# Kernel optimization log

Measured on AMD Instinct MI355X. Metric: run time of the kernel, lower is better.

Reference implementation:

```python
import math
import jax, jax.numpy as jnp
import numpy as np

# dims: layers, batch, seq, hidden, heads, ffn-mult
L, B, S, D, H, FFN = 2, 4, 2048, 256, 8, 4
HD = D // H          # head dim (= head v dim, double_v_dim=False)
EPS = 1e-5
SCALE_BASE = 512


def _ln(x, w, b):
    mu = x.mean(-1, keepdims=True)
    var = x.var(-1, keepdims=True)
    return (x - mu) * jax.lax.rsqrt(var + EPS) * w + b


def _xpos_tables():
    half = HD // 2
    sv = (np.arange(0, HD, 2) + 0.4 * HD) / (1.4 * HD)            # [half]
    pos = np.arange(S, dtype=np.float64)
    scale = sv[None, :] ** (pos[:, None] / SCALE_BASE)            # [S, half]
    inv_freq = 1.0 / (10000.0 ** (np.arange(half) / half))
    ang = pos[:, None] * inv_freq[None, :]                        # [S, half]
    return (jnp.asarray(np.sin(ang), jnp.float32),
            jnp.asarray(np.cos(ang), jnp.float32),
            jnp.asarray(scale, jnp.float32))

SIN, COS, XSCALE = _xpos_tables()


def _xpos(x, downscale=False):
    # x: [B, H, S, HD]
    sc = 1.0 / XSCALE if downscale else XSCALE
    sin2 = jnp.repeat(SIN * sc, 2, axis=-1)                       # [S, HD]
    cos2 = jnp.repeat(COS * sc, 2, axis=-1)
    x1, x2 = x[..., 0::2], x[..., 1::2]
    xr = jnp.stack((-x2, x1), axis=-1).reshape(x.shape)           # rotate_every_two
    return x * cos2 + xr * sin2


def _decay_mask():
    g = 1.0 - jnp.exp(jnp.linspace(math.log(1 / 32), math.log(1 / 512), H))
    n = jnp.arange(S)[:, None]
    m = jnp.arange(S)[None, :]
    keep = n >= m
    expo = jnp.where(keep, n - m, 0).astype(jnp.float32)
    return jnp.where(keep, g[:, None, None] ** expo[None], 0.0)   # [H, S, S]

DMASK = _decay_mask()


def setup_inputs() -> dict:
    key = jax.random.key(0)
    ks = jax.random.split(key, 16)
    sc = 1.0 / D
    f32 = jnp.float32
    return {
        "X":     jax.random.normal(ks[0], (B, S, D), f32),
        "Wq":    jax.random.normal(ks[1], (L, D, D), f32) * sc,
        "Wk":    jax.random.normal(ks[2], (L, D, D), f32) * sc,
        "Wv":    jax.random.normal(ks[3], (L, D, D), f32) * sc,
        "Wg":    jax.random.normal(ks[4], (L, D, D), f32) * sc,
        "Wo":    jax.random.normal(ks[5], (L, D, D), f32) * sc,
        "gn_w":  jnp.ones((L, D), f32) + 0.02 * jax.random.normal(ks[6], (L, D), f32),
        "gn_b":  0.02 * jax.random.normal(ks[7], (L, D), f32),
        "ln1_w": jnp.ones((L, D), f32),
        "ln1_b": jnp.zeros((L, D), f32),
        "ln2_w": jnp.ones((L, D), f32),
        "ln2_b": jnp.zeros((L, D), f32),
        "w1":    jax.random.normal(ks[8], (L, D, FFN * D), f32) * 0.02,
        "b1":    0.02 * jax.random.normal(ks[9], (L, FFN * D), f32),
        "w2":    jax.random.normal(ks[10], (L, FFN * D, D), f32) * 0.02,
        "b2":    0.02 * jax.random.normal(ks[11], (L, D), f32),
        "lnf_w": jnp.ones((D,), f32),
        "lnf_b": jnp.zeros((D,), f32),
    }


def reference(X, Wq, Wk, Wv, Wg, Wo, gn_w, gn_b, ln1_w, ln1_b,
              ln2_w, ln2_b, w1, b1, w2, b2, lnf_w, lnf_b):
    x = X
    for i in range(L):
        xn = _ln(x, ln1_w[i], ln1_b[i])                           # [B,S,D]
        q = (xn @ Wq[i]).reshape(B, S, H, HD).transpose(0, 2, 1, 3)
        k = (xn @ Wk[i]).reshape(B, S, H, HD).transpose(0, 2, 1, 3)
        v = (xn @ Wv[i]).reshape(B, S, H, HD).transpose(0, 2, 1, 3)
        q = _xpos(q)
        k = _xpos(k, downscale=True)
        att = jnp.einsum('bhnd,bhmd->bhnm', q, k) * DMASK          # [B,H,S,S]
        y = jnp.einsum('bhnm,bhmd->bhnd', att, v)                  # [B,H,S,HD]
        # GroupNorm(heads, v_dim): per-(b, position, head) normalization
        mu = y.mean(-1, keepdims=True)
        var = y.var(-1, keepdims=True)
        y = (y - mu) * jax.lax.rsqrt(var + EPS)
        y = y.transpose(0, 2, 1, 3).reshape(B, S, D)               # concat heads
        y = y * gn_w[i] + gn_b[i]
        g = xn @ Wg[i]
        ret = (g * jax.nn.sigmoid(g) * y) @ Wo[i]                  # swish gate + out proj
        yres = ret + x
        yn = _ln(yres, ln2_w[i], ln2_b[i])
        f = jax.nn.gelu(yn @ w1[i] + b1[i], approximate=False) @ w2[i] + b2[i]
        x = _ln(f + yres, lnf_w, lnf_b)
    return x
```

## Files before the change

kernel.cpp:

```cpp
#include <hip/hip_runtime.h>
#include <hip/hip_bf16.h>

typedef __hip_bfloat16 bf16;
typedef unsigned short ushort_t;
typedef __attribute__((ext_vector_type(8))) short short8v;
typedef __attribute__((ext_vector_type(4))) float f32x4;
typedef __attribute__((ext_vector_type(4))) unsigned int uint4v;

#define LYR 2
#define BB 4
#define SS 2048
#define DD 256
#define HH 8
#define HDD 32
#define FFD 1024
#define MM (BB*SS)

__device__ __forceinline__ unsigned int cvtpk(float lo, float hi) {
  unsigned int r;
  asm("v_cvt_pk_bf16_f32 %0, %1, %2" : "=v"(r) : "v"(lo), "v"(hi));
  return r;
}

__device__ __forceinline__ void gload_lds16(const void* g, void* l) {
  __builtin_amdgcn_global_load_lds((const __attribute__((address_space(1))) void*)g,
                                   (__attribute__((address_space(3))) void*)l, 16, 0, 0);
}

__device__ __forceinline__ float l2g_of(int h) {
  return log2f(1.0f - expf(-3.4657359028f - 0.3960841187f * (float)h));
}

struct WDesc { const float* src; bf16* dst; int K; int N; };
struct WDescA { WDesc d[14]; float* tsn; float* tcs; float* tsc; };
__global__ __launch_bounds__(256) void wconv_k(WDescA da) {
  if (blockIdx.z == 14) {
    int i = (blockIdx.y * 32 + blockIdx.x) * 256 + threadIdx.y * 32 + threadIdx.x;
    if (i >= SS * 16) return;
    int s = i >> 4, j = i & 15;
    float sv = (2.0f * (float)j + 0.4f * (float)HDD) / (1.4f * (float)HDD);
    da.tsc[i] = powf(sv, (float)s * (1.0f / 512.0f));
    float inv_freq = powf(10000.0f, -(float)j * (1.0f / 16.0f));
    float ang = (float)s * inv_freq;
    da.tsn[i] = sinf(ang);
    da.tcs[i] = cosf(ang);
    return;
  }
  WDesc dd = da.d[blockIdx.z];
  int n0 = blockIdx.x * 32, k0 = blockIdx.y * 32;
  if (n0 >= dd.N || k0 >= dd.K) return;
  __shared__ float t[32][33];
  int tx = threadIdx.x, ty = threadIdx.y;
  #pragma unroll
  for (int i = 0; i < 32; i += 8) t[ty + i][tx] = dd.src[(size_t)(k0 + ty + i) * dd.N + n0 + tx];
  __syncthreads();
  #pragma unroll
  for (int i = 0; i < 32; i += 8) dd.dst[(size_t)(n0 + ty + i) * dd.K + k0 + tx] = __float2bfloat16(t[tx][ty + i]);
}

template<typename OT>
__global__ __launch_bounds__(256) void ln_k(const float* __restrict__ in, const float* __restrict__ w,
    const float* __restrict__ b, OT* __restrict__ out)
{
  int row = blockIdx.x, t = threadIdx.x;
  float v = in[(size_t)row * DD + t];
  __shared__ float red[4];
  float s = v;
  #pragma unroll
  for (int m = 32; m >= 1; m >>= 1) s += __shfl_xor(s, m);
  if ((t & 63) == 0) red[t >> 6] = s;
  __syncthreads();
  float mu = (red[0] + red[1] + red[2] + red[3]) * (1.0f / 256.0f);
  float d = v - mu;
  float s2 = d * d;
  #pragma unroll
  for (int m = 32; m >= 1; m >>= 1) s2 += __shfl_xor(s2, m);
  __syncthreads();
  if ((t & 63) == 0) red[t >> 6] = s2;
  __syncthreads();
  float var = (red[0] + red[1] + red[2] + red[3]) * (1.0f / 256.0f);
  float o = d * rsqrtf(var + 1e-5f) * w[t] + b[t];
  if constexpr (sizeof(OT) == 2) out[(size_t)row * DD + t] = __float2bfloat16(o);
  else                           out[(size_t)row * DD + t] = o;
}

#define STAGEG(buf, k0s) { \
    _Pragma("unroll") \
    for (int i = 0; i < BM / 32; ++i) { \
      int slot = i * 256 + tid; int row = slot >> 3, blk = slot & 7; \
      gload_lds16(Au + (size_t)(bm + row) * K + (k0s) + ((blk ^ (row & 7))) * 8, &Al[buf][slot * 8]); \
    } \
    _Pragma("unroll") \
    for (int i = 0; i < BN / 32; ++i) { \
      int slot = i * 256 + tid; int row = slot >> 3, blk = slot & 7; \
      gload_lds16(Bu + (size_t)(bn + row) * K + (k0s) + ((blk ^ (row & 7))) * 8, &Bl[buf][slot * 8]); \
    } }

enum { E_QKVG = 0, E_BGELU = 2 };

template<int BM, int BN, int K, int EPI>
__global__ __launch_bounds__(256) void mgemm_k(const bf16* __restrict__ Ag, const bf16* __restrict__ Wt,
    const float* __restrict__ bias,
    void* o0, void* o1, void* o2, void* o3, int N,
    const float* __restrict__ tsn, const float* __restrict__ tcs, const float* __restrict__ tsc)
{
  constexpr int MT = BM / 32, NT = BN / 32;
  constexpr int WMH = BM / 2, WNH = BN / 2;
  __shared__ __align__(16) ushort_t Al[2][BM * 64];
  __shared__ __align__(16) ushort_t Bl[2][BN * 64];
  const int bm = blockIdx.x * BM;
  const int bn = blockIdx.y * BN;
  const int tid = threadIdx.x;
  const int lane = tid & 63, w = tid >> 6;
  const int lg = lane >> 4, ln = lane & 15;
  const int wr = w >> 1, wc = w & 1;
  const ushort_t* Au = (const ushort_t*)Ag;
  const ushort_t* Bu = (const ushort_t*)Wt;
  f32x4 acc[MT][NT] = {};

  STAGEG(0, 0)
  asm volatile("s_waitcnt vmcnt(0)" ::: "memory");
  __builtin_amdgcn_s_barrier();

  int cur = 0;
  for (int k0 = 0; k0 < K; k0 += 64) {
    if (k0 + 64 < K) STAGEG(cur ^ 1, k0 + 64)
    #pragma unroll
    for (int kh = 0; kh < 2; ++kh) {
      short8v af[MT], bfr[NT];
      #pragma unroll
      for (int mt = 0; mt < MT; ++mt) {
        int row = wr * WMH + mt * 16 + ln;
        af[mt] = *(const short8v*)&Al[cur][row * 64 + (((kh * 4 + lg) ^ (row & 7))) * 8];
      }
      #pragma unroll
      for (int nt = 0; nt < NT; ++nt) {
        int row = wc * WNH + nt * 16 + ln;
        bfr[nt] = *(const short8v*)&Bl[cur][row * 64 + (((kh * 4 + lg) ^ (row & 7))) * 8];
      }
      #pragma unroll
      for (int mt = 0; mt < MT; ++mt)
        #pragma unroll
        for (int nt = 0; nt < NT; ++nt)
          acc[mt][nt] = __builtin_amdgcn_mfma_f32_16x16x32_bf16(af[mt], bfr[nt], acc[mt][nt], 0, 0, 0);
    }
    asm volatile("s_waitcnt vmcnt(0)" ::: "memory");
    __builtin_amdgcn_s_barrier();
    cur ^= 1;
  }

  if constexpr (EPI == E_QKVG) {
    #pragma unroll
    for (int mt = 0; mt < MT; ++mt)
      #pragma unroll
      for (int nt = 0; nt < NT; ++nt) {
        const int colbase = bn + wc * WNH + nt * 16;
        const int sec = colbase >> 8;
        const int c = (colbase & 255) + ln;
        const int grow0 = bm + wr * WMH + mt * 16 + lg * 4;
        if (sec <= 1) {
          const int jj = (c & 31) >> 1;
          const float l2g = l2g_of(c >> 5);
          #pragma unroll
          for (int r = 0; r < 4; ++r) {
            const int grow = grow0 + r;
            const int s = grow & (SS - 1);
            float v = acc[mt][nt][r];
            float pv = __shfl_xor(v, 1);
            float scv = tsc[s * 16 + jj];
            if (sec == 1) scv = 1.0f / scv;
            float ce = tcs[s * 16 + jj] * scv, se = tsn[s * 16 + jj] * scv;
            float o = (ln & 1) ? (v * ce + pv * se) : (v * ce - pv * se);
            if (sec == 0) o *= exp2f(l2g * (float)s);
            bf16* dst = (sec == 0) ? (bf16*)o0 : (bf16*)o1;
            dst[(size_t)grow * DD + c] = __float2bfloat16(o);
          }
        } else if (sec == 2) {
          const int b = grow0 >> 11, s0 = grow0 & (SS - 1);
          const int h = c >> 5, d = c & 31;
          const float nl2g = -l2g_of(h);
          float v0 = acc[mt][nt][0] * exp2f(nl2g * (float)(s0 + 0));
          float v1 = acc[mt][nt][1] * exp2f(nl2g * (float)(s0 + 1));
          float v2 = acc[mt][nt][2] * exp2f(nl2g * (float)(s0 + 2));
          float v3 = acc[mt][nt][3] * exp2f(nl2g * (float)(s0 + 3));
          uint2 pk;
          pk.x = cvtpk(v0, v1);
          pk.y = cvtpk(v2, v3);
          *(uint2*)((ushort_t*)o2 + ((size_t)(b * 8 + h) * 32 + d) * SS + s0) = pk;
        } else {
          #pragma unroll
          for (int r = 0; r < 4; ++r)
            ((float*)o3)[(size_t)(grow0 + r) * DD + c] = acc[mt][nt][r];
        }
      }
  } else {
    #pragma unroll
    for (int mt = 0; mt < MT; ++mt)
      #pragma unroll
      for (int nt = 0; nt < NT; ++nt) {
        const int gcol = bn + wc * WNH + nt * 16 + ln;
        #pragma unroll
        for (int r = 0; r < 4; ++r) {
          const int grow = bm + wr * WMH + mt * 16 + lg * 4 + r;
          float v = acc[mt][nt][r] + bias[gcol];
          v = 0.5f * v * (1.0f + erff(v * 0.70710678118654752f));
          ((bf16*)o0)[(size_t)grow * N + gcol] = __float2bfloat16(v);
        }
      }
  }
}

template<int K, int MODE, bool LAST>
__global__ __launch_bounds__(256) void mgemm_ln(const bf16* __restrict__ Ag, const bf16* __restrict__ Wt,
    const float* __restrict__ bias, const float* __restrict__ res,
    float* __restrict__ yres, bf16* __restrict__ xn, float* __restrict__ dout,
    const float* __restrict__ law, const float* __restrict__ lab,
    const float* __restrict__ lbw, const float* __restrict__ lbb)
{
  constexpr int BM = 16;
  __shared__ __align__(16) ushort_t Al[2][BM * 64];
  __shared__ __align__(16) ushort_t Bl[2][256 * 64];
  __shared__ float red[4][16][2];
  const int bm = blockIdx.x * BM;
  const int tid = threadIdx.x;
  const int lane = tid & 63, w = tid >> 6;
  const int lg = lane >> 4, ln = lane & 15;
  const ushort_t* Au = (const ushort_t*)Ag;
  const ushort_t* Bu = (const ushort_t*)Wt;
  f32x4 acc[4] = {};

  #define STAGEL(buf, k0s) { \
    if (tid < 128) { int row = tid >> 3, blk = tid & 7; \
      gload_lds16(Au + (size_t)(bm + row) * K + (k0s) + ((blk ^ (row & 7))) * 8, &Al[buf][tid * 8]); } \
    _Pragma("unroll") \
    for (int i = 0; i < 8; ++i) { \
      int slot = i * 256 + tid; int row = slot >> 3, blk = slot & 7; \
      gload_lds16(Bu + (size_t)row * K + (k0s) + ((blk ^ (row & 7))) * 8, &Bl[buf][slot * 8]); } }

  STAGEL(0, 0)
  asm volatile("s_waitcnt vmcnt(0)" ::: "memory");
  __builtin_amdgcn_s_barrier();

  int cur = 0;
  for (int k0 = 0; k0 < K; k0 += 64) {
    if (k0 + 64 < K) STAGEL(cur ^ 1, k0 + 64)
    #pragma unroll
    for (int kh = 0; kh < 2; ++kh) {
      short8v af, bfr[4];
      af = *(const short8v*)&Al[cur][ln * 64 + (((kh * 4 + lg) ^ (ln & 7))) * 8];
      #pragma unroll
      for (int nt = 0; nt < 4; ++nt) {
        int row = w * 64 + nt * 16 + ln;
        bfr[nt] = *(const short8v*)&Bl[cur][row * 64 + (((kh * 4 + lg) ^ (row & 7))) * 8];
      }
      #pragma unroll
      for (int nt = 0; nt < 4; ++nt)
        acc[nt] = __builtin_amdgcn_mfma_f32_16x16x32_bf16(af, bfr[nt], acc[nt], 0, 0, 0);
    }
    asm volatile("s_waitcnt vmcnt(0)" ::: "memory");
    __builtin_amdgcn_s_barrier();
    cur ^= 1;
  }
  #undef STAGEL

  const int row0 = lg * 4;
  float v[4][4];
  #pragma unroll
  for (int nt = 0; nt < 4; ++nt) {
    const int gcol = w * 64 + nt * 16 + ln;
    #pragma unroll
    for (int r = 0; r < 4; ++r) {
      float t = acc[nt][r];
      if constexpr (MODE == 1) t += bias[gcol];
      t += res[(size_t)(bm + row0 + r) * DD + gcol];
      v[nt][r] = t;
    }
  }
  float mu[4], rs[4];
  {
    #pragma unroll
    for (int r = 0; r < 4; ++r) {
      float s = 0.f, s2 = 0.f;
      #pragma unroll
      for (int nt = 0; nt < 4; ++nt) { s += v[nt][r]; s2 += v[nt][r] * v[nt][r]; }
      #pragma unroll
      for (int m = 8; m >= 1; m >>= 1) { s += __shfl_xor(s, m); s2 += __shfl_xor(s2, m); }
      if (ln == 0) { red[w][row0 + r][0] = s; red[w][row0 + r][1] = s2; }
    }
    __syncthreads();
    #pragma unroll
    for (int r = 0; r < 4; ++r) {
      float S  = red[0][row0 + r][0] + red[1][row0 + r][0] + red[2][row0 + r][0] + red[3][row0 + r][0];
      float S2 = red[0][row0 + r][1] + red[1][row0 + r][1] + red[2][row0 + r][1] + red[3][row0 + r][1];
      float m_ = S * (1.0f / 256.0f);
      float var = S2 * (1.0f / 256.0f) - m_ * m_;
      mu[r] = m_; rs[r] = rsqrtf(var + 1e-5f);
    }
  }

  if constexpr (MODE == 0) {
    #pragma unroll
    for (int nt = 0; nt < 4; ++nt) {
      const int gcol = w * 64 + nt * 16 + ln;
      const float lw = law[gcol], lb = lab[gcol];
      #pragma unroll
      for (int r = 0; r < 4; ++r) {
        const size_t idx = (size_t)(bm + row0 + r) * DD + gcol;
        yres[idx] = v[nt][r];
        xn[idx] = __float2bfloat16((v[nt][r] - mu[r]) * rs[r] * lw + lb);
      }
    }
  } else {
    float u[4][4];
    #pragma unroll
    for (int nt = 0; nt < 4; ++nt) {
      const int gcol = w * 64 + nt * 16 + ln;
      const float lw = law[gcol], lb = lab[gcol];
      #pragma unroll
      for (int r = 0; r < 4; ++r)
        u[nt][r] = (v[nt][r] - mu[r]) * rs[r] * lw + lb;
    }
    if constexpr (LAST) {
      #pragma unroll
      for (int nt = 0; nt < 4; ++nt) {
        const int gcol = w * 64 + nt * 16 + ln;
        #pragma unroll
        for (int r = 0; r < 4; ++r)
          dout[(size_t)(bm + row0 + r) * DD + gcol] = u[nt][r];
      }
    } else {
      __syncthreads();
      #pragma unroll
      for (int r = 0; r < 4; ++r) {
        float s = 0.f, s2 = 0.f;
        #pragma unroll
        for (int nt = 0; nt < 4; ++nt) { s += u[nt][r]; s2 += u[nt][r] * u[nt][r]; }
        #pragma unroll
        for (int m = 8; m >= 1; m >>= 1) { s += __shfl_xor(s, m); s2 += __shfl_xor(s2, m); }
        if (ln == 0) { red[w][row0 + r][0] = s; red[w][row0 + r][1] = s2; }
      }
      __syncthreads();
      float mu2[4], rs2[4];
      #pragma unroll
      for (int r = 0; r < 4; ++r) {
        float S  = red[0][row0 + r][0] + red[1][row0 + r][0] + red[2][row0 + r][0] + red[3][row0 + r][0];
        float S2 = red[0][row0 + r][1] + red[1][row0 + r][1] + red[2][row0 + r][1] + red[3][row0 + r][1];
        float m_ = S * (1.0f / 256.0f);
        float var = S2 * (1.0f / 256.0f) - m_ * m_;
        mu2[r] = m_; rs2[r] = rsqrtf(var + 1e-5f);
      }
      #pragma unroll
      for (int nt = 0; nt < 4; ++nt) {
        const int gcol = w * 64 + nt * 16 + ln;
        const float lw = lbw[gcol], lb = lbb[gcol];
        #pragma unroll
        for (int r = 0; r < 4; ++r) {
          const size_t idx = (size_t)(bm + row0 + r) * DD + gcol;
          yres[idx] = u[nt][r];
          xn[idx] = __float2bfloat16((u[nt][r] - mu2[r]) * rs2[r] * lw + lb);
        }
      }
    }
  }
}

__global__ __launch_bounds__(256) void attn_k(const bf16* __restrict__ qg, const bf16* __restrict__ kg,
    const bf16* __restrict__ vtg, const float* __restrict__ gbuf,
    const float* __restrict__ gnw, const float* __restrict__ gnb, bf16* __restrict__ ub)
{
  __shared__ __align__(16) ushort_t Kl[2][64 * 32];
  __shared__ __align__(16) ushort_t Vl[2][32 * 64];
  __shared__ __align__(16) unsigned int Pl[4][512];

  const int bh = blockIdx.x;
  const int b = bh >> 3, h = bh & (HH - 1);
  const int n0 = ((int)gridDim.y - 1 - (int)blockIdx.y) * 64;
  const int tid = threadIdx.x;
  const int w = tid >> 6, lane = tid & 63;
  const int lg = lane >> 4, ln = lane & 15;

  const size_t base = (size_t)b * SS * DD + h * HDD;
  const ushort_t* qp = (const ushort_t*)qg + base;
  const ushort_t* kp = (const ushort_t*)kg + base;
  const ushort_t* vtp = (const ushort_t*)vtg + (size_t)(b * 8 + h) * 32 * SS;

  const int n = n0 + w * 16 + ln;
  const short8v qf = *(const short8v*)(qp + (size_t)n * DD + lg * 8);

  const float l2g = l2g_of(h);
  f32x4 acc0 = {0,0,0,0}, acc1 = {0,0,0,0};

  const int Wwin = (int)(20.0f / (-l2g)) + 1;
  int m_lo = 0;
  if (n0 > Wwin) m_lo = ((n0 - Wwin) >> 6) << 6;

  const int Krow = tid >> 2, Kc8 = tid & 3;
  const int Vrow = tid >> 3, Vc8 = tid & 7;

  #define STAGE(buf, m0s) { \
    gload_lds16(kp + (size_t)((m0s) + Krow) * DD + ((Kc8 ^ (Krow & 3)) * 8), &Kl[buf][tid * 8]); \
    gload_lds16(vtp + (size_t)Vrow * SS + (m0s) + ((Vc8 ^ (Vrow & 7)) * 8), &Vl[buf][tid * 8]); }

  STAGE(0, m_lo)
  asm volatile("s_waitcnt vmcnt(0)" ::: "memory");
  __builtin_amdgcn_s_barrier();

  int cur = 0;
  for (int m0 = m_lo; m0 <= n0; m0 += 64) {
    if (m0 < n0) STAGE(cur ^ 1, m0 + 64)
    const bool diag = (m0 == n0);
    __builtin_amdgcn_s_setprio(1);
    #pragma unroll
    for (int mt = 0; mt < 4; ++mt) {
      const int krow = mt * 16 + ln;
      short8v kf = *(const short8v*)&Kl[cur][krow * 32 + ((lg ^ (krow & 3)) << 3)];
      f32x4 z = {0,0,0,0};
      f32x4 pa = __builtin_amdgcn_mfma_f32_16x16x32_bf16(kf, qf, z, 0, 0, 0);
      float v0 = pa[0], v1 = pa[1], v2 = pa[2], v3 = pa[3];
      if (diag) {
        const int m = n0 + mt * 16 + lg * 4;
        v0 = (n < m)     ? 0.f : v0;
        v1 = (n < m + 1) ? 0.f : v1;
        v2 = (n < m + 2) ? 0.f : v2;
        v3 = (n < m + 3) ? 0.f : v3;
      }
      uint2 pk;
      pk.x = cvtpk(v0, v1);
      pk.y = cvtpk(v2, v3);
      const int blk = (mt * 2 + (lg >> 1)) ^ (ln & 7);
      *(uint2*)&Pl[w][ln * 32 + blk * 4 + (lg & 1) * 2] = pk;
    }
    #pragma unroll
    for (int hh = 0; hh < 2; ++hh) {
      const int pblk = (hh * 4 + lg) ^ (ln & 7);
      uint4v pw = *(const uint4v*)&Pl[w][ln * 32 + pblk * 4];
      short8v pf = __builtin_bit_cast(short8v, pw);
      #pragma unroll
      for (int dt = 0; dt < 2; ++dt) {
        const int d = dt * 16 + ln;
        short8v vf = *(const short8v*)&Vl[cur][d * 64 + (((hh * 4 + lg) ^ (d & 7)) << 3)];
        if (dt == 0) acc0 = __builtin_amdgcn_mfma_f32_16x16x32_bf16(vf, pf, acc0, 0, 0, 0);
        else         acc1 = __builtin_amdgcn_mfma_f32_16x16x32_bf16(vf, pf, acc1, 0, 0, 0);
      }
    }
    __builtin_amdgcn_s_setprio(0);
    asm volatile("s_waitcnt vmcnt(0)" ::: "memory");
    __builtin_amdgcn_s_barrier();
    cur ^= 1;
  }
  #undef STAGE

  float gwv[8], gbv[8];
  #pragma unroll
  for (int dt = 0; dt < 2; ++dt) {
    f32x4 a = *(const f32x4*)&gnw[h * 32 + dt * 16 + lg * 4];
    f32x4 c = *(const f32x4*)&gnb[h * 32 + dt * 16 + lg * 4];
    #pragma unroll
    for (int r = 0; r < 4; ++r) { gwv[dt * 4 + r] = a[r]; gbv[dt * 4 + r] = c[r]; }
  }
  float s = 0.f;
  #pragma unroll
  for (int r = 0; r < 4; ++r) s += acc0[r] + acc1[r];
  s += __shfl_xor(s, 16); s += __shfl_xor(s, 32);
  const float mu = s * (1.0f / 32.0f);
  float s2 = 0.f;
  #pragma unroll
  for (int r = 0; r < 4; ++r) { float d0 = acc0[r] - mu, d1 = acc1[r] - mu; s2 += d0 * d0 + d1 * d1; }
  s2 += __shfl_xor(s2, 16); s2 += __shfl_xor(s2, 32);
  const float rs = rsqrtf(s2 * (1.0f / 32.0f) + 1e-5f);
  const size_t rowoff = ((size_t)b * SS + n) * DD + h * 32;
  #pragma unroll
  for (int dt = 0; dt < 2; ++dt) {
    f32x4 yv = dt ? acc1 : acc0;
    f32x4 gv = *(const f32x4*)&gbuf[rowoff + dt * 16 + lg * 4];
    float o0, o1, o2, o3;
    {
      float yn0 = (yv[0] - mu) * rs * gwv[dt * 4 + 0] + gbv[dt * 4 + 0];
      float yn1 = (yv[1] - mu) * rs * gwv[dt * 4 + 1] + gbv[dt * 4 + 1];
      float yn2 = (yv[2] - mu) * rs * gwv[dt * 4 + 2] + gbv[dt * 4 + 2];
      float yn3 = (yv[3] - mu) * rs * gwv[dt * 4 + 3] + gbv[dt * 4 + 3];
      o0 = gv[0] / (1.0f + expf(-gv[0])) * yn0;
      o1 = gv[1] / (1.0f + expf(-gv[1])) * yn1;
      o2 = gv[2] / (1.0f + expf(-gv[2])) * yn2;
      o3 = gv[3] / (1.0f + expf(-gv[3])) * yn3;
    }
    uint2 pk;
    pk.x = cvtpk(o0, o1);
    pk.y = cvtpk(o2, o3);
    *(uint2*)((ushort_t*)ub + rowoff + dt * 16 + lg * 4) = pk;
  }
}

extern "C" void kernel_launch(void* const* d_in, const int* in_sizes, int n_in,
                              void* d_out, int out_size, void* d_ws, size_t ws_size,
                              hipStream_t stream)
{
  const float* X    = (const float*)d_in[0];
  const float* Wq   = (const float*)d_in[1];
  const float* Wk   = (const float*)d_in[2];
  const float* Wv   = (const float*)d_in[3];
  const float* Wg   = (const float*)d_in[4];
  const float* Wo   = (const float*)d_in[5];
  const float* gnw  = (const float*)d_in[6];
  const float* gnb  = (const float*)d_in[7];
  const float* ln1w = (const float*)d_in[8];
  const float* ln1b = (const float*)d_in[9];
  const float* ln2w = (const float*)d_in[10];
  const float* ln2b = (const float*)d_in[11];
  const float* w1   = (const float*)d_in[12];
  const float* b1   = (const float*)d_in[13];
  const float* w2   = (const float*)d_in[14];
  const float* b2   = (const float*)d_in[15];
  const float* lnfw = (const float*)d_in[16];
  const float* lnfb = (const float*)d_in[17];

  char* p = (char*)d_ws;
  const size_t AF  = (size_t)MM * DD * sizeof(float);
  const size_t ABF = (size_t)MM * DD * sizeof(bf16);
  bf16*  xn   = (bf16*)p;  p += ABF;
  bf16*  qb   = (bf16*)p;  p += ABF;
  bf16*  kb   = (bf16*)p;  p += ABF;
  bf16*  vT   = (bf16*)p;  p += ABF;
  bf16*  ub   = (bf16*)p;  p += ABF;
  float* gbuf = (float*)p; p += AF;
  float* yres = (float*)p; p += AF;
  bf16*  wqkvgt = (bf16*)p; p += (size_t)2 * 1024 * 256 * sizeof(bf16);
  bf16*  wot    = (bf16*)p; p += (size_t)2 * 256 * 256 * sizeof(bf16);
  bf16*  w1t    = (bf16*)p; p += (size_t)2 * 1024 * 256 * sizeof(bf16);
  bf16*  w2t    = (bf16*)p; p += (size_t)2 * 256 * 1024 * sizeof(bf16);
  float* tsn  = (float*)p; p += SS * 16 * sizeof(float);
  float* tcs  = (float*)p; p += SS * 16 * sizeof(float);
  float* tsc  = (float*)p; p += SS * 16 * sizeof(float);
  bf16*  h1   = qb;

  {
    WDescA da;
    for (int l = 0; l < 2; ++l) {
      da.d[l * 7 + 0] = { Wq + (size_t)l * 65536, wqkvgt + (size_t)l * 262144 + 0 * 65536, 256, 256 };
      da.d[l * 7 + 1] = { Wk + (size_t)l * 65536, wqkvgt + (size_t)l * 262144 + 1 * 65536, 256, 256 };
      da.d[l * 7 + 2] = { Wv + (size_t)l * 65536, wqkvgt + (size_t)l * 262144 + 2 * 65536, 256, 256 };
      da.d[l * 7 + 3] = { Wg + (size_t)l * 65536, wqkvgt + (size_t)l * 262144 + 3 * 65536, 256, 256 };
      da.d[l * 7 + 4] = { Wo + (size_t)l * 65536, wot + (size_t)l * 65536, 256, 256 };
      da.d[l * 7 + 5] = { w1 + (size_t)l * 262144, w1t + (size_t)l * 262144, 256, 1024 };
      da.d[l * 7 + 6] = { w2 + (size_t)l * 262144, w2t + (size_t)l * 262144, 1024, 256 };
    }
    da.tsn = tsn; da.tcs = tcs; da.tsc = tsc;
    wconv_k<<<dim3(32, 32, 15), dim3(32, 8), 0, stream>>>(da);
  }

  ln_k<bf16><<<dim3(MM), 256, 0, stream>>>(X, ln1w, ln1b, xn);

  for (int l = 0; l < LYR; ++l) {
    mgemm_k<64, 128, DD, E_QKVG><<<dim3(MM / 64, 1024 / 128), 256, 0, stream>>>(
        xn, wqkvgt + (size_t)l * 262144, nullptr, qb, kb, vT, gbuf, 1024, tsn, tcs, tsc);
    attn_k<<<dim3(BB * HH, SS / 64), 256, 0, stream>>>(qb, kb, vT, gbuf, gnw + l * DD, gnb + l * DD, ub);
    mgemm_ln<DD, 0, false><<<dim3(MM / 16), 256, 0, stream>>>(
        ub, wot + (size_t)l * 65536, nullptr, (l == 0) ? X : yres, yres, xn, nullptr,
        ln2w + l * DD, ln2b + l * DD, nullptr, nullptr);
    mgemm_k<64, 128, DD, E_BGELU><<<dim3(MM / 64, FFD / 128), 256, 0, stream>>>(
        xn, w1t + (size_t)l * 262144, b1 + l * FFD, h1, nullptr, nullptr, nullptr, FFD, tsn, tcs, tsc);
    if (l == LYR - 1) {
      mgemm_ln<FFD, 1, true><<<dim3(MM / 16), 256, 0, stream>>>(
          h1, w2t + (size_t)l * 262144, b2 + l * DD, yres, nullptr, nullptr, (float*)d_out,
          lnfw, lnfb, nullptr, nullptr);
    } else {
      mgemm_ln<FFD, 1, false><<<dim3(MM / 16), 256, 0, stream>>>(
          h1, w2t + (size_t)l * 262144, b2 + l * DD, yres, yres, xn, nullptr,
          lnfw, lnfb, ln1w + (l + 1) * DD, ln1b + (l + 1) * DD);
    }
  }
}
```

Before: 200.5 us.

## Fuse out-projection, LN2, FFN up/GELU/down and final LNs into one kernel

New measurement: 200.6 us. Within noise of the previous version (+0.0%).

```diff
diff --git a/kernel.cpp b/kernel.cpp
--- a/kernel.cpp
+++ b/kernel.cpp
@@ -21,6 +21,7 @@
   asm("v_cvt_pk_bf16_f32 %0, %1, %2" : "=v"(r) : "v"(lo), "v"(hi));
   return r;
 }
+__device__ __forceinline__ ushort_t f2b1(float x) { return (ushort_t)cvtpk(x, x); }
 
 __device__ __forceinline__ void gload_lds16(const void* g, void* l) {
   __builtin_amdgcn_global_load_lds((const __attribute__((address_space(1))) void*)g,
@@ -96,12 +97,11 @@
       gload_lds16(Bu + (size_t)(bn + row) * K + (k0s) + ((blk ^ (row & 7))) * 8, &Bl[buf][slot * 8]); \
     } }
 
-enum { E_QKVG = 0, E_BGELU = 2 };
+enum { E_QKVG = 0 };
 
 template<int BM, int BN, int K, int EPI>
 __global__ __launch_bounds__(256) void mgemm_k(const bf16* __restrict__ Ag, const bf16* __restrict__ Wt,
-    const float* __restrict__ bias,
-    void* o0, void* o1, void* o2, void* o3, int N,
+    void* o0, void* o1, void* o2, void* o3,
     const float* __restrict__ tsn, const float* __restrict__ tcs, const float* __restrict__ tsc)
 {
   constexpr int MT = BM / 32, NT = BN / 32;
@@ -149,219 +149,297 @@
     cur ^= 1;
   }
 
-  if constexpr (EPI == E_QKVG) {
-    #pragma unroll
-    for (int mt = 0; mt < MT; ++mt)
-      #pragma unroll
-      for (int nt = 0; nt < NT; ++nt) {
-        const int colbase = bn + wc * WNH + nt * 16;
-        const int sec = colbase >> 8;
-        const int c = (colbase & 255) + ln;
-        const int grow0 = bm + wr * WMH + mt * 16 + lg * 4;
-        if (sec <= 1) {
-          const int jj = (c & 31) >> 1;
-          const float l2g = l2g_of(c >> 5);
-          #pragma unroll
-          for (int r = 0; r < 4; ++r) {
-            const int grow = grow0 + r;
-            const int s = grow & (SS - 1);
-            float v = acc[mt][nt][r];
-            float pv = __shfl_xor(v, 1);
-            float scv = tsc[s * 16 + jj];
-            if (sec == 1) scv = 1.0f / scv;
-            float ce = tcs[s * 16 + jj] * scv, se = tsn[s * 16 + jj] * scv;
-            float o = (ln & 1) ? (v * ce + pv * se) : (v * ce - pv * se);
-            if (sec == 0) o *= exp2f(l2g * (float)s);
-            bf16* dst = (sec == 0) ? (bf16*)o0 : (bf16*)o1;
-            dst[(size_t)grow * DD + c] = __float2bfloat16(o);
-          }
-        } else if (sec == 2) {
-          const int b = grow0 >> 11, s0 = grow0 & (SS - 1);
-          const int h = c >> 5, d = c & 31;
-          const float nl2g = -l2g_of(h);
-          float v0 = acc[mt][nt][0] * exp2f(nl2g * (float)(s0 + 0));
-          float v1 = acc[mt][nt][1] * exp2f(nl2g * (float)(s0 + 1));
-          float v2 = acc[mt][nt][2] * exp2f(nl2g * (float)(s0 + 2));
-          float v3 = acc[mt][nt][3] * exp2f(nl2g * (float)(s0 + 3));
-          uint2 pk;
-          pk.x = cvtpk(v0, v1);
-          pk.y = cvtpk(v2, v3);
-          *(uint2*)((ushort_t*)o2 + ((size_t)(b * 8 + h) * 32 + d) * SS + s0) = pk;
-        } else {
-          #pragma unroll
-          for (int r = 0; r < 4; ++r)
-            ((float*)o3)[(size_t)(grow0 + r) * DD + c] = acc[mt][nt][r];
-        }
-      }
-  } else {
-    #pragma unroll
-    for (int mt = 0; mt < MT; ++mt)
-      #pragma unroll
-      for (int nt = 0; nt < NT; ++nt) {
-        const int gcol = bn + wc * WNH + nt * 16 + ln;
+  #pragma unroll
+  for (int mt = 0; mt < MT; ++mt)
+    #pragma unroll
+    for (int nt = 0; nt < NT; ++nt) {
+      const int colbase = bn + wc * WNH + nt * 16;
+      const int sec = colbase >> 8;
+      const int c = (colbase & 255) + ln;
+      const int grow0 = bm + wr * WMH + mt * 16 + lg * 4;
+      if (sec <= 1) {
+        const int jj = (c & 31) >> 1;
+        const float l2g = l2g_of(c >> 5);
         #pragma unroll
         for (int r = 0; r < 4; ++r) {
-          const int grow = bm + wr * WMH + mt * 16 + lg * 4 + r;
-          float v = acc[mt][nt][r] + bias[gcol];
-          v = 0.5f * v * (1.0f + erff(v * 0.70710678118654752f));
-          ((bf16*)o0)[(size_t)grow * N + gcol] = __float2bfloat16(v);
+          const int grow = grow0 + r;
+          const int s = grow & (SS - 1);
+          float v = acc[mt][nt][r];
+          float pv = __shfl_xor(v, 1);
+          float scv = tsc[s * 16 + jj];
+          if (sec == 1) scv = 1.0f / scv;
+          float ce = tcs[s * 16 + jj] * scv, se = tsn[s * 16 + jj] * scv;
+          float o = (ln & 1) ? (v * ce + pv * se) : (v * ce - pv * se);
+          if (sec == 0) o *= exp2f(l2g * (float)s);
+          bf16* dst = (sec == 0) ? (bf16*)o0 : (bf16*)o1;
+          dst[(size_t)grow * DD + c] = __float2bfloat16(o);
         }
-      }
-  }
-}
-
-template<int K, int MODE, bool LAST>
-__global__ __launch_bounds__(256) void mgemm_ln(const bf16* __restrict__ Ag, const bf16* __restrict__ Wt,
-    const float* __restrict__ bias, const float* __restrict__ res,
+      } else if (sec == 2) {
+        const int b = grow0 >> 11, s0 = grow0 & (SS - 1);
+        const int h = c >> 5, d = c & 31;
+        const float nl2g = -l2g_of(h);
+        float v0 = acc[mt][nt][0] * exp2f(nl2g * (float)(s0 + 0));
+        float v1 = acc[mt][nt][1] * exp2f(nl2g * (float)(s0 + 1));
+        float v2 = acc[mt][nt][2] * exp2f(nl2g * (float)(s0 + 2));
+        float v3 = acc[mt][nt][3] * exp2f(nl2g * (float)(s0 + 3));
+        uint2 pk;
+        pk.x = cvtpk(v0, v1);
+        pk.y = cvtpk(v2, v3);
+        *(uint2*)((ushort_t*)o2 + ((size_t)(b * 8 + h) * 32 + d) * SS + s0) = pk;
+      } else {
+        #pragma unroll
+        for (int r = 0; r < 4; ++r)
+          ((float*)o3)[(size_t)(grow0 + r) * DD + c] = acc[mt][nt][r];
+      }
+    }
+}
+
+template<bool LAST>
+__global__ __launch_bounds__(256) void ffn_mega(
+    const bf16* __restrict__ ubg, const bf16* __restrict__ wotg,
+    const bf16* __restrict__ w1tg, const bf16* __restrict__ w2tg,
+    const float* __restrict__ b1v, const float* __restrict__ b2v,
+    const float* __restrict__ resin,
     float* __restrict__ yres, bf16* __restrict__ xn, float* __restrict__ dout,
-    const float* __restrict__ law, const float* __restrict__ lab,
-    const float* __restrict__ lbw, const float* __restrict__ lbb)
+    const float* __restrict__ l2w, const float* __restrict__ l2b,
+    const float* __restrict__ lfw, const float* __restrict__ lfb,
+    const float* __restrict__ l1w, const float* __restrict__ l1b)
 {
-  constexpr int BM = 16;
-  __shared__ __align__(16) ushort_t Al[2][BM * 64];
-  __shared__ __align__(16) ushort_t Bl[2][256 * 64];
-  __shared__ float red[4][16][2];
-  const int bm = blockIdx.x * BM;
+  __shared__ __align__(16) ushort_t Bs[2][256 * 64];
+  __shared__ __align__(16) ushort_t AX[4096];
+  __shared__ __align__(16) ushort_t Us[4096];
+
+  const int bm = blockIdx.x * 16;
   const int tid = threadIdx.x;
   const int lane = tid & 63, w = tid >> 6;
   const int lg = lane >> 4, ln = lane & 15;
-  const ushort_t* Au = (const ushort_t*)Ag;
-  const ushort_t* Bu = (const ushort_t*)Wt;
-  f32x4 acc[4] = {};
-
-  #define STAGEL(buf, k0s) { \
-    if (tid < 128) { int row = tid >> 3, blk = tid & 7; \
-      gload_lds16(Au + (size_t)(bm + row) * K + (k0s) + ((blk ^ (row & 7))) * 8, &Al[buf][tid * 8]); } \
+  const int row0 = lg * 4;
+  const ushort_t* ubu  = (const ushort_t*)ubg;
+  const ushort_t* wotu = (const ushort_t*)wotg;
+  const ushort_t* w1tu = (const ushort_t*)w1tg;
+  const ushort_t* w2tu = (const ushort_t*)w2tg;
+  float* red = (float*)Us;
+
+  float resv[4][4];
+  #pragma unroll
+  for (int nt = 0; nt < 4; ++nt) {
+    const int gcol = w * 64 + nt * 16 + ln;
+    #pragma unroll
+    for (int r = 0; r < 4; ++r)
+      resv[nt][r] = resin[(size_t)(bm + row0 + r) * DD + gcol];
+  }
+
+  #define STAGEB(buf, base, stride, koff) { \
     _Pragma("unroll") \
     for (int i = 0; i < 8; ++i) { \
       int slot = i * 256 + tid; int row = slot >> 3, blk = slot & 7; \
-      gload_lds16(Bu + (size_t)row * K + (k0s) + ((blk ^ (row & 7))) * 8, &Bl[buf][slot * 8]); } }
-
-  STAGEL(0, 0)
-  asm volatile("s_waitcnt vmcnt(0)" ::: "memory");
-  __builtin_amdgcn_s_barrier();
-
+      gload_lds16((base) + (size_t)row * (stride) + (koff) + ((blk ^ (row & 7))) * 8, &Bs[buf][slot * 8]); \
+    } }
+  #define STAGEA(buf, koff) { \
+    if (tid < 128) { int row = tid >> 3, blk = tid & 7; \
+      gload_lds16(ubu + (size_t)(bm + row) * DD + (koff) + ((blk ^ (row & 7))) * 8, &AX[(buf) * 1024 + tid * 8]); } }
+  #define DRAIN asm volatile("s_waitcnt vmcnt(0)" ::: "memory"); __builtin_amdgcn_s_barrier();
+
+  STAGEA(0, 0)
+  STAGEB(0, wotu, 256, 0)
+  DRAIN
   int cur = 0;
-  for (int k0 = 0; k0 < K; k0 += 64) {
-    if (k0 + 64 < K) STAGEL(cur ^ 1, k0 + 64)
+
+  f32x4 accw[4] = {};
+  #pragma unroll
+  for (int s = 0; s < 4; ++s) {
+    if (s < 3) { STAGEA(cur ^ 1, (s + 1) * 64) STAGEB(cur ^ 1, wotu, 256, (s + 1) * 64) }
+    else       { STAGEB(cur ^ 1, w1tu, 256, 0) }
     #pragma unroll
     for (int kh = 0; kh < 2; ++kh) {
-      short8v af, bfr[4];
-      af = *(const short8v*)&Al[cur][ln * 64 + (((kh * 4 + lg) ^ (ln & 7))) * 8];
+      short8v af = *(const short8v*)&AX[cur * 1024 + ln * 64 + (((kh * 4 + lg) ^ (ln & 7))) * 8];
       #pragma unroll
       for (int nt = 0; nt < 4; ++nt) {
         int row = w * 64 + nt * 16 + ln;
-        bfr[nt] = *(const short8v*)&Bl[cur][row * 64 + (((kh * 4 + lg) ^ (row & 7))) * 8];
-      }
-      #pragma unroll
-      for (int nt = 0; nt < 4; ++nt)
-        acc[nt] = __builtin_amdgcn_mfma_f32_16x16x32_bf16(af, bfr[nt], acc[nt], 0, 0, 0);
-    }
-    asm volatile("s_waitcnt vmcnt(0)" ::: "memory");
-    __builtin_amdgcn_s_barrier();
+        short8v bf_ = *(const short8v*)&Bs[cur][row * 64 + (((kh * 4 + lg) ^ (row & 7))) * 8];
+        accw[nt] = __builtin_amdgcn_mfma_f32_16x16x32_bf16(af, bf_, accw[nt], 0, 0, 0);
+      }
+    }
+    DRAIN
     cur ^= 1;
   }
-  #undef STAGEL
-
-  const int row0 = lg * 4;
+
   float v[4][4];
+  #pragma unroll
+  for (int nt = 0; nt < 4; ++nt)
+    #pragma unroll
+    for (int r = 0; r < 4; ++r) v[nt][r] = accw[nt][r] + resv[nt][r];
+  float mu[4], rsg[4];
+  {
+    #pragma unroll
+    for (int r = 0; r < 4; ++r) {
+      float s1 = 0.f, s2 = 0.f;
+      #pragma unroll
+      for (int nt = 0; nt < 4; ++nt) { s1 += v[nt][r]; s2 += v[nt][r] * v[nt][r]; }
+      #pragma unroll
+      for (int m = 8; m >= 1; m >>= 1) { s1 += __shfl_xor(s1, m); s2 += __shfl_xor(s2, m); }
+      if (ln == 0) { red[(w * 16 + row0 + r) * 2] = s1; red[(w * 16 + row0 + r) * 2 + 1] = s2; }
+    }
+    __syncthreads();
+    #pragma unroll
+    for (int r = 0; r < 4; ++r) {
+      float S = 0.f, S2 = 0.f;
+      #pragma unroll
+      for (int ww = 0; ww < 4; ++ww) { S += red[(ww * 16 + row0 + r) * 2]; S2 += red[(ww * 16 + row0 + r) * 2 + 1]; }
+      float m_ = S * (1.0f / 256.0f);
+      mu[r] = m_; rsg[r] = rsqrtf(S2 * (1.0f / 256.0f) - m_ * m_ + 1e-5f);
+    }
+  }
+  __syncthreads();
   #pragma unroll
   for (int nt = 0; nt < 4; ++nt) {
     const int gcol = w * 64 + nt * 16 + ln;
+    const float lwv = l2w[gcol], lbv = l2b[gcol];
+    const int off = nt * 16 + ln, blk = off >> 3, sub = off & 7;
     #pragma unroll
     for (int r = 0; r < 4; ++r) {
-      float t = acc[nt][r];
-      if constexpr (MODE == 1) t += bias[gcol];
-      t += res[(size_t)(bm + row0 + r) * DD + gcol];
-      v[nt][r] = t;
-    }
-  }
-  float mu[4], rs[4];
+      const int row = row0 + r;
+      float xv = (v[nt][r] - mu[r]) * rsg[r] * lwv + lbv;
+      AX[row * 256 + w * 64 + ((blk ^ (row & 7)) << 3) + sub] = f2b1(xv);
+    }
+  }
+  __syncthreads();
+
+  f32x4 acc2[4] = {};
+  #pragma unroll
+  for (int c = 0; c < 4; ++c) {
+    f32x4 acc1[4] = {};
+    #pragma unroll
+    for (int s = 0; s < 4; ++s) {
+      if (s < 3) { STAGEB(cur ^ 1, w1tu + (size_t)c * 65536, 256, (s + 1) * 64) }
+      else       { STAGEB(cur ^ 1, w2tu + c * 256, 1024, 0) }
+      #pragma unroll
+      for (int kh = 0; kh < 2; ++kh) {
+        short8v af = *(const short8v*)&AX[ln * 256 + s * 64 + (((kh * 4 + lg) ^ (ln & 7))) * 8];
+        #pragma unroll
+        for (int nt = 0; nt < 4; ++nt) {
+          int row = w * 64 + nt * 16 + ln;
+          short8v bf_ = *(const short8v*)&Bs[cur][row * 64 + (((kh * 4 + lg) ^ (row & 7))) * 8];
+          acc1[nt] = __builtin_amdgcn_mfma_f32_16x16x32_bf16(af, bf_, acc1[nt], 0, 0, 0);
+        }
+      }
+      DRAIN
+      cur ^= 1;
+    }
+    #pragma unroll
+    for (int nt = 0; nt < 4; ++nt) {
+      const int gcol1 = c * 256 + w * 64 + nt * 16 + ln;
+      const float bb = b1v[gcol1];
+      const int off = nt * 16 + ln, blk = off >> 3, sub = off & 7;
+      #pragma unroll
+      for (int r = 0; r < 4; ++r) {
+        const int row = row0 + r;
+        float t = acc1[nt][r] + bb;
+        t = 0.5f * t * (1.0f + erff(t * 0.70710678118654752f));
+        Us[row * 256 + w * 64 + ((blk ^ (row & 7)) << 3) + sub] = f2b1(t);
+      }
+    }
+    __syncthreads();
+    #pragma unroll
+    for (int s = 0; s < 4; ++s) {
+      if (s < 3)      { STAGEB(cur ^ 1, w2tu + c * 256, 1024, (s + 1) * 64) }
+      else if (c < 3) { STAGEB(cur ^ 1, w1tu + (size_t)(c + 1) * 65536, 256, 0) }
+      #pragma unroll
+      for (int kh = 0; kh < 2; ++kh) {
+        short8v af = *(const short8v*)&Us[ln * 256 + s * 64 + (((kh * 4 + lg) ^ (ln & 7))) * 8];
+        #pragma unroll
+        for (int nt = 0; nt < 4; ++nt) {
+          int row = w * 64 + nt * 16 + ln;
+          short8v bf_ = *(const short8v*)&Bs[cur][row * 64 + (((kh * 4 + lg) ^ (row & 7))) * 8];
+          acc2[nt] = __builtin_amdgcn_mfma_f32_16x16x32_bf16(af, bf_, acc2[nt], 0, 0, 0);
+        }
+      }
+      DRAIN
+      cur ^= 1;
+    }
+  }
+
+  float f[4][4];
+  #pragma unroll
+  for (int nt = 0; nt < 4; ++nt) {
+    const int gcol = w * 64 + nt * 16 + ln;
+    const float bb = b2v[gcol];
+    #pragma unroll
+    for (int r = 0; r < 4; ++r) f[nt][r] = acc2[nt][r] + bb + v[nt][r];
+  }
   {
     #pragma unroll
     for (int r = 0; r < 4; ++r) {
-      float s = 0.f, s2 = 0.f;
-      #pragma unroll
-      for (int nt = 0; nt < 4; ++nt) { s += v[nt][r]; s2 += v[nt][r] * v[nt][r]; }
-      #pragma unroll
-      for (int m = 8; m >= 1; m >>= 1) { s += __shfl_xor(s, m); s2 += __shfl_xor(s2, m); }
-      if (ln == 0) { red[w][row0 + r][0] = s; red[w][row0 + r][1] = s2; }
+      float s1 = 0.f, s2 = 0.f;
+      #pragma unroll
+      for (int nt = 0; nt < 4; ++nt) { s1 += f[nt][r]; s2 += f[nt][r] * f[nt][r]; }
+      #pragma unroll
+      for (int m = 8; m >= 1; m >>= 1) { s1 += __shfl_xor(s1, m); s2 += __shfl_xor(s2, m); }
+      if (ln == 0) { red[(w * 16 + row0 + r) * 2] = s1; red[(w * 16 + row0 + r) * 2 + 1] = s2; }
     }
     __syncthreads();
     #pragma unroll
     for (int r = 0; r < 4; ++r) {
-      float S  = red[0][row0 + r][0] + red[1][row0 + r][0] + red[2][row0 + r][0] + red[3][row0 + r][0];
-      float S2 = red[0][row0 + r][1] + red[1][row0 + r][1] + red[2][row0 + r][1] + red[3][row0 + r][1];
+      float S = 0.f, S2 = 0.f;
+      #pragma unroll
+      for (int ww = 0; ww < 4; ++ww) { S += red[(ww * 16 + row0 + r) * 2]; S2 += red[(ww * 16 + row0 + r) * 2 + 1]; }
       float m_ = S * (1.0f / 256.0f);
-      float var = S2 * (1.0f / 256.0f) - m_ * m_;
-      mu[r] = m_; rs[r] = rsqrtf(var + 1e-5f);
-    }
-  }
-
-  if constexpr (MODE == 0) {
+      mu[r] = m_; rsg[r] = rsqrtf(S2 * (1.0f / 256.0f) - m_ * m_ + 1e-5f);
+    }
+  }
+  float u[4][4];
+  #pragma unroll
+  for (int nt = 0; nt < 4; ++nt) {
+    const int gcol = w * 64 + nt * 16 + ln;
+    const float lwv = lfw[gcol], lbv = lfb[gcol];
+    #pragma unroll
+    for (int r = 0; r < 4; ++r)
+      u[nt][r] = (f[nt][r] - mu[r]) * rsg[r] * lwv + lbv;
+  }
+  if constexpr (LAST) {
     #pragma unroll
     for (int nt = 0; nt < 4; ++nt) {
       const int gcol = w * 64 + nt * 16 + ln;
-      const float lw = law[gcol], lb = lab[gcol];
+      #pragma unroll
+      for (int r = 0; r < 4; ++r)
+        dout[(size_t)(bm + row0 + r) * DD + gcol] = u[nt][r];
+    }
+  } else {
+    __syncthreads();
+    #pragma unroll
+    for (int r = 0; r < 4; ++r) {
+      float s1 = 0.f, s2 = 0.f;
+      #pragma unroll
+      for (int nt = 0; nt < 4; ++nt) { s1 += u[nt][r]; s2 += u[nt][r] * u[nt][r]; }
+      #pragma unroll
+      for (int m = 8; m >= 1; m >>= 1) { s1 += __shfl_xor(s1, m); s2 += __shfl_xor(s2, m); }
+      if (ln == 0) { red[(w * 16 + row0 + r) * 2] = s1; red[(w * 16 + row0 + r) * 2 + 1] = s2; }
+    }
+    __syncthreads();
+    float mu2[4], rs2[4];
+    #pragma unroll
+    for (int r = 0; r < 4; ++r) {
+      float S = 0.f, S2 = 0.f;
+      #pragma unroll
+      for (int ww = 0; ww < 4; ++ww) { S += red[(ww * 16 + row0 + r) * 2]; S2 += red[(ww * 16 + row0 + r) * 2 + 1]; }
+      float m_ = S * (1.0f / 256.0f);
+      mu2[r] = m_; rs2[r] = rsqrtf(S2 * (1.0f / 256.0f) - m_ * m_ + 1e-5f);
+    }
+    #pragma unroll
+    for (int nt = 0; nt < 4; ++nt) {
+      const int gcol = w * 64 + nt * 16 + ln;
+      const float lwv = l1w[gcol], lbv = l1b[gcol];
       #pragma unroll
       for (int r = 0; r < 4; ++r) {
         const size_t idx = (size_t)(bm + row0 + r) * DD + gcol;
-        yres[idx] = v[nt][r];
-        xn[idx] = __float2bfloat16((v[nt][r] - mu[r]) * rs[r] * lw + lb);
-      }
-    }
-  } else {
-    float u[4][4];
-    #pragma unroll
-    for (int nt = 0; nt < 4; ++nt) {
-      const int gcol = w * 64 + nt * 16 + ln;
-      const float lw = law[gcol], lb = lab[gcol];
-      #pragma unroll
-      for (int r = 0; r < 4; ++r)
-        u[nt][r] = (v[nt][r] - mu[r]) * rs[r] * lw + lb;
-    }
-    if constexpr (LAST) {
-      #pragma unroll
-      for (int nt = 0; nt < 4; ++nt) {
-        const int gcol = w * 64 + nt * 16 + ln;
-        #pragma unroll
-        for (int r = 0; r < 4; ++r)
-          dout[(size_t)(bm + row0 + r) * DD + gcol] = u[nt][r];
-      }
-    } else {
-      __syncthreads();
-      #pragma unroll
-      for (int r = 0; r < 4; ++r) {
-        float s = 0.f, s2 = 0.f;
-        #pragma unroll
-        for (int nt = 0; nt < 4; ++nt) { s += u[nt][r]; s2 += u[nt][r] * u[nt][r]; }
-        #pragma unroll
-        for (int m = 8; m >= 1; m >>= 1) { s += __shfl_xor(s, m); s2 += __shfl_xor(s2, m); }
-        if (ln == 0) { red[w][row0 + r][0] = s; red[w][row0 + r][1] = s2; }
-      }
-      __syncthreads();
-      float mu2[4], rs2[4];
-      #pragma unroll
-      for (int r = 0; r < 4; ++r) {
-        float S  = red[0][row0 + r][0] + red[1][row0 + r][0] + red[2][row0 + r][0] + red[3][row0 + r][0];
-        float S2 = red[0][row0 + r][1] + red[1][row0 + r][1] + red[2][row0 + r][1] + red[3][row0 + r][1];
-        float m_ = S * (1.0f / 256.0f);
-        float var = S2 * (1.0f / 256.0f) - m_ * m_;
-        mu2[r] = m_; rs2[r] = rsqrtf(var + 1e-5f);
-      }
-      #pragma unroll
-      for (int nt = 0; nt < 4; ++nt) {
-        const int gcol = w * 64 + nt * 16 + ln;
-        const float lw = lbw[gcol], lb = lbb[gcol];
-        #pragma unroll
-        for (int r = 0; r < 4; ++r) {
-          const size_t idx = (size_t)(bm + row0 + r) * DD + gcol;
-          yres[idx] = u[nt][r];
-          xn[idx] = __float2bfloat16((u[nt][r] - mu2[r]) * rs2[r] * lw + lb);
-        }
-      }
-    }
-  }
+        yres[idx] = u[nt][r];
+        xn[idx] = __float2bfloat16((u[nt][r] - mu2[r]) * rs2[r] * lwv + lbv);
+      }
+    }
+  }
+  #undef STAGEB
+  #undef STAGEA
+  #undef DRAIN
 }
 
 __global__ __launch_bounds__(256) void attn_k(const bf16* __restrict__ qg, const bf16* __restrict__ kg,
@@ -531,7 +609,6 @@
   float* tsn  = (float*)p; p += SS * 16 * sizeof(float);
   float* tcs  = (float*)p; p += SS * 16 * sizeof(float);
   float* tsc  = (float*)p; p += SS * 16 * sizeof(float);
-  bf16*  h1   = qb;
 
   {
     WDescA da;
@@ -552,21 +629,20 @@
 
   for (int l = 0; l < LYR; ++l) {
     mgemm_k<64, 128, DD, E_QKVG><<<dim3(MM / 64, 1024 / 128), 256, 0, stream>>>(
-        xn, wqkvgt + (size_t)l * 262144, nullptr, qb, kb, vT, gbuf, 1024, tsn, tcs, tsc);
+        xn, wqkvgt + (size_t)l * 262144, qb, kb, vT, gbuf, tsn, tcs, tsc);
     attn_k<<<dim3(BB * HH, SS / 64), 256, 0, stream>>>(qb, kb, vT, gbuf, gnw + l * DD, gnb + l * DD, ub);
-    mgemm_ln<DD, 0, false><<<dim3(MM / 16), 256, 0, stream>>>(
-        ub, wot + (size_t)l * 65536, nullptr, (l == 0) ? X : yres, yres, xn, nullptr,
-        ln2w + l * DD, ln2b + l * DD, nullptr, nullptr);
-    mgemm_k<64, 128, DD, E_BGELU><<<dim3(MM / 64, FFD / 128), 256, 0, stream>>>(
-        xn, w1t + (size_t)l * 262144, b1 + l * FFD, h1, nullptr, nullptr, nullptr, FFD, tsn, tcs, tsc);
     if (l == LYR - 1) {
-      mgemm_ln<FFD, 1, true><<<dim3(MM / 16), 256, 0, stream>>>(
-          h1, w2t + (size_t)l * 262144, b2 + l * DD, yres, nullptr, nullptr, (float*)d_out,
-          lnfw, lnfb, nullptr, nullptr);
+      ffn_mega<true><<<dim3(MM / 16), 256, 0, stream>>>(
+          ub, wot + (size_t)l * 65536, w1t + (size_t)l * 262144, w2t + (size_t)l * 262144,
+          b1 + l * FFD, b2 + l * DD, (l == 0) ? X : yres,
+          nullptr, nullptr, (float*)d_out,
+          ln2w + l * DD, ln2b + l * DD, lnfw, lnfb, nullptr, nullptr);
     } else {
-      mgemm_ln<FFD, 1, false><<<dim3(MM / 16), 256, 0, stream>>>(
-          h1, w2t + (size_t)l * 262144, b2 + l * DD, yres, yres, xn, nullptr,
-          lnfw, lnfb, ln1w + (l + 1) * DD, ln1b + (l + 1) * DD);
-    }
-  }
-}
+      ffn_mega<false><<<dim3(MM / 16), 256, 0, stream>>>(
+          ub, wot + (size_t)l * 65536, w1t + (size_t)l * 262144, w2t + (size_t)l * 262144,
+          b1 + l * FFD, b2 + l * DD, (l == 0) ? X : yres,
+          yres, xn, nullptr,
+          ln2w + l * DD, ln2b + l * DD, lnfw, lnfb, ln1w + (l + 1) * DD, ln1b + (l + 1) * DD);
+    }
+  }
+}
```
